# Optimization experiments

Measured on AMD Instinct MI355X. Metric: run time of the kernel, lower is better.

## Reference

```python
import jax, jax.numpy as jnp
import numpy as np

IMG_H, IMG_W = 448, 800
GRID = 224
MIN_SIZE = 64.0
B, N, NCAM = 1, 48, 6


def setup_inputs() -> dict:
    rng = np.random.default_rng(0)
    centers = np.stack([rng.uniform(-40, 40, (B, N)), rng.uniform(-40, 40, (B, N)),
                        rng.uniform(-1.5, 0.5, (B, N))], -1)
    dims = rng.uniform(1.0, 4.0, (B, N, 3))
    heading = rng.uniform(-np.pi, np.pi, (B, N, 1))
    boxes7 = np.concatenate([centers, dims, heading], -1).astype(np.float32)
    gt_labels = rng.integers(1, 11, (B, N)).astype(np.int64)  # 1..10 as in gt_boxes[...,-1]
    imgs = rng.random((B, NCAM, 3, IMG_H, IMG_W)).astype(np.float32)
    # plausible lidar->image projections: 6 outward-facing cams, 60 deg apart, 90 deg hfov
    fx = fy = 400.0
    K = np.array([[fx, 0, IMG_W / 2], [0, fy, IMG_H / 2], [0, 0, 1]], np.float32)
    l2i = np.zeros((B, NCAM, 4, 4), np.float32)
    for c in range(NCAM):
        th = 2 * np.pi * c / NCAM
        right = np.array([np.sin(th), -np.cos(th), 0.0])
        down = np.array([0.0, 0.0, -1.0])
        fwdv = np.array([np.cos(th), np.sin(th), 0.0])
        R = np.stack([right, down, fwdv])  # lidar -> cam
        l2i[:, c, :3, :3] = K @ R
        l2i[:, c, 3, 3] = 1.0
    eye4 = np.eye(4, dtype=np.float32)
    img_aug = np.broadcast_to(eye4, (B, NCAM, 4, 4)).copy()
    lidar_aug = np.broadcast_to(eye4, (B, 4, 4)).copy()
    W_img = (rng.standard_normal((588, 768)) * 0.02).astype(np.float32)
    text_features = rng.standard_normal((10, 768)).astype(np.float32)
    return dict(boxes7=jnp.asarray(boxes7), gt_labels=jnp.asarray(gt_labels),
                camera_imgs=jnp.asarray(imgs), lidar2image=jnp.asarray(l2i),
                img_aug_matrix=jnp.asarray(img_aug), lidar_aug_matrix=jnp.asarray(lidar_aug),
                W_img=jnp.asarray(W_img), text_features=jnp.asarray(text_features),
                logit_scale=jnp.asarray(np.float32(np.log(100.0))))


def _boxes_to_corners_3d(boxes7):  # (M,7) -> (M,8,3)
    template = jnp.array([[1, 1, -1], [1, -1, -1], [-1, -1, -1], [-1, 1, -1],
                          [1, 1, 1], [1, -1, 1], [-1, -1, 1], [-1, 1, 1]], jnp.float32) * 0.5
    corners = boxes7[:, None, 3:6] * template[None]
    c, s = jnp.cos(boxes7[:, 6]), jnp.sin(boxes7[:, 6])
    z, o = jnp.zeros_like(c), jnp.ones_like(c)
    rot = jnp.stack([c, s, z, -s, c, z, z, z, o], -1).reshape(-1, 3, 3)
    corners = jnp.einsum('nki,nij->nkj', corners, rot)  # points @ R as in torch code
    return corners + boxes7[:, None, :3]


def _project(corners, l2i, img_aug, lidar_aug):
    # corners (M,3); l2i/img_aug (6,4,4); lidar_aug (4,4)
    pts = corners - lidar_aug[:3, 3]
    pts = jnp.linalg.inv(lidar_aug[:3, :3]) @ pts.T  # (3,M)
    p = jnp.einsum('cij,jm->cim', l2i[:, :3, :3], pts) + l2i[:, :3, 3][:, :, None]
    zc = jnp.clip(p[:, 2], 1e-5, 1e5)
    xy = p[:, :2] / zc[:, None]
    p = jnp.concatenate([xy, zc[:, None]], axis=1)  # (6,3,M)
    p = jnp.einsum('cij,cjm->cim', img_aug[:, :3, :3], p) + img_aug[:, :3, 3][:, :, None]
    rc = p[:, :2].transpose(0, 2, 1)[..., ::-1]  # (6,M,2) as (row, col)
    on_img = (rc[..., 0] < IMG_H) & (rc[..., 0] >= 0) & (rc[..., 1] < IMG_W) & (rc[..., 1] >= 0)
    return rc, on_img


def _bilinear(img, ix, iy):
    # img (3,H,W); ix, iy (N,GRID,GRID) pixel coords; zero padding, align_corners=False
    x0f, y0f = jnp.floor(ix), jnp.floor(iy)
    wx1, wy1 = ix - x0f, iy - y0f
    wx0, wy0 = 1.0 - wx1, 1.0 - wy1

    def gather(xf, yf):
        valid = (xf >= 0) & (xf <= IMG_W - 1) & (yf >= 0) & (yf <= IMG_H - 1)
        xi = jnp.clip(xf.astype(jnp.int32), 0, IMG_W - 1)
        yi = jnp.clip(yf.astype(jnp.int32), 0, IMG_H - 1)
        return img[:, yi, xi] * valid[None].astype(img.dtype)  # (3,N,G,G)

    return (gather(x0f, y0f) * (wx0 * wy0)[None] + gather(x0f + 1, y0f) * (wx1 * wy0)[None]
            + gather(x0f, y0f + 1) * (wx0 * wy1)[None] + gather(x0f + 1, y0f + 1) * (wx1 * wy1)[None])


def _forward(boxes7, gt_labels, camera_imgs, lidar2image, img_aug_matrix,
             lidar_aug_matrix, W_img, text_features, logit_scale):
    Bx, Nx = boxes7.shape[:2]
    corners = _boxes_to_corners_3d(boxes7.reshape(-1, 7)).reshape(Bx, Nx * 8, 3)
    rc, on_img = jax.vmap(_project)(corners, lidar2image, img_aug_matrix, lidar_aug_matrix)
    # .long() in torch truncates toward zero; coords are constants wrt grads
    all_coords = jax.lax.stop_gradient(jnp.trunc(rc)).astype(jnp.int32).reshape(Bx, NCAM, Nx, 8, 2)
    visible = on_img.reshape(Bx, NCAM, Nx, 8).any(-1)  # (B,6,N)
    rows, cols = all_coords[..., 0], all_coords[..., 1]
    x1 = jnp.clip(cols.min(-1), 0, IMG_W)
    x2 = jnp.clip(cols.max(-1), 0, IMG_W)
    y1 = jnp.clip(rows.min(-1), 0, IMG_H)
    y2 = jnp.clip(rows.max(-1), 0, IMG_H)
    sq = jnp.maximum(jnp.maximum(x2 - x1, y2 - y1).astype(jnp.float32), MIN_SIZE)
    u = jnp.linspace(0.0, 1.0, GRID)  # normalized affine_grid after min/max rescale
    px = x1.astype(jnp.float32)[..., None, None] + sq[..., None, None] * u[None, None, None, None, :]
    py = y1.astype(jnp.float32)[..., None, None] + sq[..., None, None] * u[None, None, None, :, None]
    gx = px / IMG_W * 2.0 - 1.0
    gy = py / IMG_H * 2.0 - 1.0
    ix = ((gx + 1.0) * IMG_W - 1.0) / 2.0  # unnormalize (align_corners=False)
    iy = ((gy + 1.0) * IMG_H - 1.0) / 2.0
    patches = jax.vmap(jax.vmap(_bilinear))(camera_imgs, ix, iy)  # (B,6,3,N,G,G)
    patches = patches.transpose(0, 1, 3, 2, 4, 5)  # (B,6,N,3,G,G)
    # stub CLIP image tower: 16x16 avg pool -> flatten -> linear to 768
    pooled = patches.reshape(Bx, NCAM, Nx, 3, 14, 16, 14, 16).mean(axis=(5, 7))
    feats = pooled.reshape(Bx, NCAM, Nx, 588) @ W_img  # (B,6,N,768)
    feats = feats / jnp.linalg.norm(feats, axis=-1, keepdims=True)
    text_n = text_features / jnp.linalg.norm(text_features, axis=-1, keepdims=True)
    logits = jnp.exp(logit_scale) * jnp.einsum('bcnd,kd->bcnk', feats, text_n)
    probs = jax.nn.softmax(logits, axis=-1) * visible[..., None].astype(logits.dtype)
    cnt = visible.sum(1).astype(probs.dtype)  # (B,N) cameras per box
    mean_probs = probs.sum(1) / jnp.maximum(cnt, 1.0)[..., None]  # (B,N,10)
    pred = jnp.argmax(mean_probs, axis=-1).reshape(-1)
    true = gt_labels.reshape(-1) - 1
    acc = (pred == true).astype(jnp.float32).mean()
    return pred, true, acc, mean_probs


def reference(boxes7, gt_labels, camera_imgs, lidar2image, img_aug_matrix,
              lidar_aug_matrix, W_img, text_features, logit_scale):
    return _forward(boxes7, gt_labels, camera_imgs, lidar2image, img_aug_matrix,
                    lidar_aug_matrix, W_img, text_features, logit_scale)
```

## Files before the change

kernel.cpp:

```cpp
#include <hip/hip_runtime.h>
#include <math.h>

#define IMG_H 448
#define IMG_W 800
#define GRIDN 224
#define NCAM 6
#define NBOX 48
#define NPAIR (NCAM * NBOX)
#define NCLASS 10
#define FEATD 768
#define POOLD 588
#define PROWS 14
#define KSPLIT 4
#define KCH 147

#define WS_PAIR 0
#define WS_TNORM (NPAIR * 4)
#define WS_POOL (WS_TNORM + NCLASS)
#define WS_FEAT (WS_POOL + NPAIR * POOLD)
#define WS_PROBS (WS_FEAT + NPAIR * KSPLIT * FEATD)

__global__ void prep_kernel(const float* __restrict__ boxes7,
                            const float* __restrict__ l2i,
                            const float* __restrict__ img_aug,
                            const float* __restrict__ lidar_aug,
                            const float* __restrict__ text,
                            float* __restrict__ ws) {
    int tid = threadIdx.x;
    if (tid < NCLASS) {
        float s = 0.f;
        for (int d = 0; d < FEATD; ++d) { float v = text[tid * FEATD + d]; s += v * v; }
        ws[WS_TNORM + tid] = sqrtf(s);
    }
    if (tid >= NPAIR) return;
    int cam = tid / NBOX, box = tid % NBOX;

    float R[9];
    for (int i = 0; i < 3; ++i)
        for (int j = 0; j < 3; ++j) R[i * 3 + j] = lidar_aug[i * 4 + j];
    float ltx = lidar_aug[3], lty = lidar_aug[7], ltz = lidar_aug[11];
    float det = R[0] * (R[4] * R[8] - R[5] * R[7]) - R[1] * (R[3] * R[8] - R[5] * R[6]) +
                R[2] * (R[3] * R[7] - R[4] * R[6]);
    float inv[9];
    inv[0] = (R[4] * R[8] - R[5] * R[7]) / det;
    inv[1] = (R[2] * R[7] - R[1] * R[8]) / det;
    inv[2] = (R[1] * R[5] - R[2] * R[4]) / det;
    inv[3] = (R[5] * R[6] - R[3] * R[8]) / det;
    inv[4] = (R[0] * R[8] - R[2] * R[6]) / det;
    inv[5] = (R[2] * R[3] - R[0] * R[5]) / det;
    inv[6] = (R[3] * R[7] - R[4] * R[6]) / det;
    inv[7] = (R[1] * R[6] - R[0] * R[7]) / det;
    inv[8] = (R[0] * R[4] - R[1] * R[3]) / det;

    const float* M = l2i + cam * 16;
    const float* A = img_aug + cam * 16;
    const float* bx = boxes7 + box * 7;
    float cx = bx[0], cy = bx[1], cz = bx[2];
    float dx = bx[3], dy = bx[4], dz = bx[5], hd = bx[6];
    float ch = cosf(hd), sh = sinf(hd);
    const float tmpl[8][3] = {{.5f, .5f, -.5f},  {.5f, -.5f, -.5f}, {-.5f, -.5f, -.5f},
                              {-.5f, .5f, -.5f}, {.5f, .5f, .5f},   {.5f, -.5f, .5f},
                              {-.5f, -.5f, .5f}, {-.5f, .5f, .5f}};
    int minr = 0x7FFFFFFF, maxr = -0x7FFFFFFF - 1;
    int minc = 0x7FFFFFFF, maxc = -0x7FFFFFFF - 1;
    bool vis = false;
    for (int k = 0; k < 8; ++k) {
        float lx = dx * tmpl[k][0], ly = dy * tmpl[k][1], lz = dz * tmpl[k][2];
        float wxr = lx * ch - ly * sh;
        float wyr = lx * sh + ly * ch;
        float wzr = lz;
        float wx = wxr + cx, wy = wyr + cy, wz = wzr + cz;
        float px_ = wx - ltx, py_ = wy - lty, pz_ = wz - ltz;
        float qx = inv[0] * px_ + inv[1] * py_ + inv[2] * pz_;
        float qy = inv[3] * px_ + inv[4] * py_ + inv[5] * pz_;
        float qz = inv[6] * px_ + inv[7] * py_ + inv[8] * pz_;
        float p0 = M[0] * qx + M[1] * qy + M[2] * qz + M[3];
        float p1 = M[4] * qx + M[5] * qy + M[6] * qz + M[7];
        float p2 = M[8] * qx + M[9] * qy + M[10] * qz + M[11];
        float zc = fminf(fmaxf(p2, 1e-5f), 1e5f);
        float sx = p0 / zc, sy = p1 / zc;
        float q0 = A[0] * sx + A[1] * sy + A[2] * zc + A[3];
        float q1 = A[4] * sx + A[5] * sy + A[6] * zc + A[7];
        float row = q1, col = q0;
        bool on = (row < (float)IMG_H) && (row >= 0.f) && (col < (float)IMG_W) && (col >= 0.f);
        vis = vis || on;
        int ri = (int)row;
        int ci = (int)col;
        minr = min(minr, ri); maxr = max(maxr, ri);
        minc = min(minc, ci); maxc = max(maxc, ci);
    }
    int x1 = min(max(minc, 0), IMG_W);
    int x2 = min(max(maxc, 0), IMG_W);
    int y1 = min(max(minr, 0), IMG_H);
    int y2 = min(max(maxr, 0), IMG_H);
    int side = max(x2 - x1, y2 - y1);
    float sq = fmaxf((float)side, 64.0f);
    float* pw = ws + WS_PAIR + tid * 4;
    pw[0] = (float)x1;
    pw[1] = (float)y1;
    pw[2] = sq;
    pw[3] = vis ? 1.0f : 0.0f;
}

__global__ void __launch_bounds__(256) pool_kernel(const float* __restrict__ imgs,
                                                   float* __restrict__ ws) {
    int pair = blockIdx.x / PROWS;
    int pr = blockIdx.x % PROWS;
    const float* pw = ws + WS_PAIR + pair * 4;
    if (pw[3] == 0.f) return;
    float bx1 = pw[0], by1 = pw[1], sq = pw[2];
    int cam = pair / NBOX;
    const float* img = imgs + (size_t)cam * 3 * IMG_H * IMG_W;
    int tid = threadIdx.x;
    bool active = tid < GRIDN;

    const float ustep = 1.0f / 223.0f;
    float wx0 = 0.f, wx1 = 0.f, mx0 = 0.f, mx1 = 0.f;
    int xi0 = 0, xi1 = 0;
    if (active) {
        float u = (float)tid * ustep;
        float px = bx1 + sq * u;
        float gx = px / (float)IMG_W * 2.0f - 1.0f;
        float ix = ((gx + 1.0f) * (float)IMG_W - 1.0f) / 2.0f;
        float x0f = floorf(ix);
        wx1 = ix - x0f;
        wx0 = 1.0f - wx1;
        float x1f = x0f + 1.0f;
        mx0 = (x0f >= 0.f && x0f <= (float)(IMG_W - 1)) ? 1.f : 0.f;
        mx1 = (x1f >= 0.f && x1f <= (float)(IMG_W - 1)) ? 1.f : 0.f;
        xi0 = min(max((int)x0f, 0), IMG_W - 1);
        xi1 = min(max((int)x1f, 0), IMG_W - 1);
    }
    float acc0 = 0.f, acc1 = 0.f, acc2 = 0.f;
    for (int r = 0; r < 16; ++r) {
        int i = pr * 16 + r;
        float u = (float)i * ustep;
        float py = by1 + sq * u;
        float gy = py / (float)IMG_H * 2.0f - 1.0f;
        float iy = ((gy + 1.0f) * (float)IMG_H - 1.0f) / 2.0f;
        float y0f = floorf(iy);
        float wy1 = iy - y0f;
        float wy0 = 1.0f - wy1;
        float y1f = y0f + 1.0f;
        float my0 = (y0f >= 0.f && y0f <= (float)(IMG_H - 1)) ? 1.f : 0.f;
        float my1 = (y1f >= 0.f && y1f <= (float)(IMG_H - 1)) ? 1.f : 0.f;
        int yi0 = min(max((int)y0f, 0), IMG_H - 1);
        int yi1 = min(max((int)y1f, 0), IMG_H - 1);
        if (active) {
            int r0 = yi0 * IMG_W, r1 = yi1 * IMG_W;
            float w00 = wx0 * wy0, w10 = wx1 * wy0, w01 = wx0 * wy1, w11 = wx1 * wy1;
            float m00 = mx0 * my0, m10 = mx1 * my0, m01 = mx0 * my1, m11 = mx1 * my1;
            {
                const float* ip = img;
                float v = ip[r0 + xi0] * m00 * w00 + ip[r0 + xi1] * m10 * w10 +
                          ip[r1 + xi0] * m01 * w01 + ip[r1 + xi1] * m11 * w11;
                acc0 += v;
            }
            {
                const float* ip = img + (size_t)(IMG_H * IMG_W);
                float v = ip[r0 + xi0] * m00 * w00 + ip[r0 + xi1] * m10 * w10 +
                          ip[r1 + xi0] * m01 * w01 + ip[r1 + xi1] * m11 * w11;
                acc1 += v;
            }
            {
                const float* ip = img + (size_t)(2 * IMG_H * IMG_W);
                float v = ip[r0 + xi0] * m00 * w00 + ip[r0 + xi1] * m10 * w10 +
                          ip[r1 + xi0] * m01 * w01 + ip[r1 + xi1] * m11 * w11;
                acc2 += v;
            }
        }
    }
    for (int off = 8; off >= 1; off >>= 1) {
        acc0 += __shfl_xor(acc0, off, 16);
        acc1 += __shfl_xor(acc1, off, 16);
        acc2 += __shfl_xor(acc2, off, 16);
    }
    if (active && (tid & 15) == 0) {
        int pj = tid >> 4;
        float* pool = ws + WS_POOL + (size_t)pair * POOLD;
        pool[0 * 196 + pr * 14 + pj] = acc0 * (1.0f / 256.0f);
        pool[1 * 196 + pr * 14 + pj] = acc1 * (1.0f / 256.0f);
        pool[2 * 196 + pr * 14 + pj] = acc2 * (1.0f / 256.0f);
    }
}

__global__ void __launch_bounds__(768) head1_kernel(const float* __restrict__ W,
                                                    float* __restrict__ ws) {
    int pair = blockIdx.x / KSPLIT;
    int kc = blockIdx.x % KSPLIT;
    if (ws[WS_PAIR + pair * 4 + 3] == 0.f) return;
    int tid = threadIdx.x;
    __shared__ float pk[KCH];
    if (tid < KCH) pk[tid] = ws[WS_POOL + (size_t)pair * POOLD + kc * KCH + tid];
    __syncthreads();
    const float* Wp = W + (size_t)(kc * KCH) * FEATD + tid;
    float f = 0.f;
#pragma unroll 7
    for (int k = 0; k < KCH; ++k) f += pk[k] * Wp[(size_t)k * FEATD];
    ws[WS_FEAT + ((size_t)pair * KSPLIT + kc) * FEATD + tid] = f;
}

__global__ void __launch_bounds__(256) head2_kernel(const float* __restrict__ text,
                                                    const float* __restrict__ ls_ptr,
                                                    float* __restrict__ ws) {
    int pair = blockIdx.x;
    int tid = threadIdx.x;
    const float* pw = ws + WS_PAIR + pair * 4;
    if (pw[3] == 0.f) {
        if (tid < NCLASS) ws[WS_PROBS + pair * NCLASS + tid] = 0.f;
        return;
    }
    const float* fb = ws + WS_FEAT + (size_t)pair * KSPLIT * FEATD;
    float f0 = 0.f, f1 = 0.f, f2 = 0.f;
    for (int kc = 0; kc < KSPLIT; ++kc) {
        const float* fp = fb + (size_t)kc * FEATD;
        f0 += fp[tid];
        f1 += fp[tid + 256];
        f2 += fp[tid + 512];
    }
    float pn = f0 * f0 + f1 * f1 + f2 * f2;
    float pl[NCLASS];
    for (int k = 0; k < NCLASS; ++k) {
        const float* tr = text + (size_t)k * FEATD;
        pl[k] = f0 * tr[tid] + f1 * tr[tid + 256] + f2 * tr[tid + 512];
    }
    for (int off = 32; off >= 1; off >>= 1) {
        pn += __shfl_xor(pn, off);
        for (int k = 0; k < NCLASS; ++k) pl[k] += __shfl_xor(pl[k], off);
    }
    __shared__ float rn[4];
    __shared__ float rl[4][NCLASS];
    int wave = tid >> 6, lane = tid & 63;
    if (lane == 0) {
        rn[wave] = pn;
        for (int k = 0; k < NCLASS; ++k) rl[wave][k] = pl[k];
    }
    __syncthreads();
    if (tid == 0) {
        float n2 = rn[0] + rn[1] + rn[2] + rn[3];
        float nrm = sqrtf(n2);
        float scale = expf(ls_ptr[0]);
        const float* tn = ws + WS_TNORM;
        float lg[NCLASS], m = -1e30f;
        for (int k = 0; k < NCLASS; ++k) {
            float d = rl[0][k] + rl[1][k] + rl[2][k] + rl[3][k];
            lg[k] = scale * (d / (nrm * tn[k]));
            m = fmaxf(m, lg[k]);
        }
        float s = 0.f;
        for (int k = 0; k < NCLASS; ++k) {
            lg[k] = expf(lg[k] - m);
            s += lg[k];
        }
        float* probs = ws + WS_PROBS + pair * NCLASS;
        for (int k = 0; k < NCLASS; ++k) probs[k] = lg[k] / s;
    }
}

__global__ void finalize_kernel(const int* __restrict__ gt, const float* __restrict__ ws,
                                float* __restrict__ out) {
    int n = threadIdx.x;
    bool match = false;
    if (n < NBOX) {
        const float* probs = ws + WS_PROBS;
        float cnt = 0.f;
        for (int c = 0; c < NCAM; ++c)
            cnt += (ws[WS_PAIR + (c * NBOX + n) * 4 + 3] != 0.f) ? 1.f : 0.f;
        float denom = fmaxf(cnt, 1.0f);
        float mp[NCLASS];
        for (int k = 0; k < NCLASS; ++k) {
            float s = 0.f;
            for (int c = 0; c < NCAM; ++c) s += probs[(c * NBOX + n) * NCLASS + k];
            mp[k] = s / denom;
            out[97 + n * NCLASS + k] = mp[k];
        }
        float best = mp[0];
        int pred = 0;
        for (int k = 1; k < NCLASS; ++k)
            if (mp[k] > best) { best = mp[k]; pred = k; }
        int tr = gt[n] - 1;
        out[n] = (float)pred;
        out[NBOX + n] = (float)tr;
        match = (pred == tr);
    }
    unsigned long long b = __ballot(match);
    if (n == 0) out[2 * NBOX] = (float)__popcll(b) / (float)NBOX;
}

extern "C" void kernel_launch(void* const* d_in, const int* in_sizes, int n_in,
                              void* d_out, int out_size, void* d_ws, size_t ws_size,
                              hipStream_t stream) {
    const float* boxes7 = (const float*)d_in[0];
    const int* gt = (const int*)d_in[1];
    const float* imgs = (const float*)d_in[2];
    const float* l2i = (const float*)d_in[3];
    const float* img_aug = (const float*)d_in[4];
    const float* lidar_aug = (const float*)d_in[5];
    const float* W = (const float*)d_in[6];
    const float* text = (const float*)d_in[7];
    const float* ls = (const float*)d_in[8];
    float* ws = (float*)d_ws;
    float* out = (float*)d_out;

    prep_kernel<<<1, 320, 0, stream>>>(boxes7, l2i, img_aug, lidar_aug, text, ws);
    pool_kernel<<<NPAIR * PROWS, 256, 0, stream>>>(imgs, ws);
    head1_kernel<<<NPAIR * KSPLIT, 768, 0, stream>>>(W, ws);
    head2_kernel<<<NPAIR, 256, 0, stream>>>(text, ls, ws);
    finalize_kernel<<<1, 64, 0, stream>>>(gt, ws, out);
}
```

Measured before the change: 54.31 us.

## Fuse box projection into pool kernel and fold text norms into head2

Removes the single-block prep kernel. Each pool block now projects its box's 8 corners itself, using 8 lanes and a shuffle min/max reduction, and the text norms are computed inside head2 alongside the dot products. The pool kernel grows to 1024 threads, with four row groups of 4 rows each reduced through shared memory, so each block has more parallelism. This saves a launch and the serial prep step. In exchange, the projection is computed redundantly in all 14 blocks per pair, and invisible pairs still launch large blocks that exit early.

```diff
diff --git a/kernel.cpp b/kernel.cpp
--- a/kernel.cpp
+++ b/kernel.cpp
@@ -15,65 +15,59 @@
 #define KCH 147
 
 #define WS_PAIR 0
-#define WS_TNORM (NPAIR * 4)
-#define WS_POOL (WS_TNORM + NCLASS)
+#define WS_POOL (NPAIR * 4)
 #define WS_FEAT (WS_POOL + NPAIR * POOLD)
 #define WS_PROBS (WS_FEAT + NPAIR * KSPLIT * FEATD)
 
-__global__ void prep_kernel(const float* __restrict__ boxes7,
-                            const float* __restrict__ l2i,
-                            const float* __restrict__ img_aug,
-                            const float* __restrict__ lidar_aug,
-                            const float* __restrict__ text,
-                            float* __restrict__ ws) {
+__global__ void __launch_bounds__(1024) pool_kernel(const float* __restrict__ imgs,
+                                                    const float* __restrict__ boxes7,
+                                                    const float* __restrict__ l2i,
+                                                    const float* __restrict__ img_aug,
+                                                    const float* __restrict__ lidar_aug,
+                                                    float* __restrict__ ws) {
+    int pair = blockIdx.x / PROWS;
+    int pr = blockIdx.x % PROWS;
+    int cam = pair / NBOX, box = pair % NBOX;
     int tid = threadIdx.x;
-    if (tid < NCLASS) {
-        float s = 0.f;
-        for (int d = 0; d < FEATD; ++d) { float v = text[tid * FEATD + d]; s += v * v; }
-        ws[WS_TNORM + tid] = sqrtf(s);
-    }
-    if (tid >= NPAIR) return;
-    int cam = tid / NBOX, box = tid % NBOX;
-
-    float R[9];
-    for (int i = 0; i < 3; ++i)
-        for (int j = 0; j < 3; ++j) R[i * 3 + j] = lidar_aug[i * 4 + j];
-    float ltx = lidar_aug[3], lty = lidar_aug[7], ltz = lidar_aug[11];
-    float det = R[0] * (R[4] * R[8] - R[5] * R[7]) - R[1] * (R[3] * R[8] - R[5] * R[6]) +
-                R[2] * (R[3] * R[7] - R[4] * R[6]);
-    float inv[9];
-    inv[0] = (R[4] * R[8] - R[5] * R[7]) / det;
-    inv[1] = (R[2] * R[7] - R[1] * R[8]) / det;
-    inv[2] = (R[1] * R[5] - R[2] * R[4]) / det;
-    inv[3] = (R[5] * R[6] - R[3] * R[8]) / det;
-    inv[4] = (R[0] * R[8] - R[2] * R[6]) / det;
-    inv[5] = (R[2] * R[3] - R[0] * R[5]) / det;
-    inv[6] = (R[3] * R[7] - R[4] * R[6]) / det;
-    inv[7] = (R[1] * R[6] - R[0] * R[7]) / det;
-    inv[8] = (R[0] * R[4] - R[1] * R[3]) / det;
-
-    const float* M = l2i + cam * 16;
-    const float* A = img_aug + cam * 16;
-    const float* bx = boxes7 + box * 7;
-    float cx = bx[0], cy = bx[1], cz = bx[2];
-    float dx = bx[3], dy = bx[4], dz = bx[5], hd = bx[6];
-    float ch = cosf(hd), sh = sinf(hd);
-    const float tmpl[8][3] = {{.5f, .5f, -.5f},  {.5f, -.5f, -.5f}, {-.5f, -.5f, -.5f},
-                              {-.5f, .5f, -.5f}, {.5f, .5f, .5f},   {.5f, -.5f, .5f},
-                              {-.5f, -.5f, .5f}, {-.5f, .5f, .5f}};
-    int minr = 0x7FFFFFFF, maxr = -0x7FFFFFFF - 1;
-    int minc = 0x7FFFFFFF, maxc = -0x7FFFFFFF - 1;
-    bool vis = false;
-    for (int k = 0; k < 8; ++k) {
-        float lx = dx * tmpl[k][0], ly = dy * tmpl[k][1], lz = dz * tmpl[k][2];
-        float wxr = lx * ch - ly * sh;
-        float wyr = lx * sh + ly * ch;
-        float wzr = lz;
-        float wx = wxr + cx, wy = wyr + cy, wz = wzr + cz;
+
+    __shared__ float s_pw[4];
+    __shared__ float s_part[4][3][14];
+
+    if (tid < 64) {
+        int k = tid & 7;
+        float R[9];
+        for (int i = 0; i < 3; ++i)
+            for (int j = 0; j < 3; ++j) R[i * 3 + j] = lidar_aug[i * 4 + j];
+        float ltx = lidar_aug[3], lty = lidar_aug[7], ltz = lidar_aug[11];
+        float det = R[0] * (R[4] * R[8] - R[5] * R[7]) - R[1] * (R[3] * R[8] - R[5] * R[6]) +
+                    R[2] * (R[3] * R[7] - R[4] * R[6]);
+        float i0 = (R[4] * R[8] - R[5] * R[7]) / det;
+        float i1 = (R[2] * R[7] - R[1] * R[8]) / det;
+        float i2 = (R[1] * R[5] - R[2] * R[4]) / det;
+        float i3 = (R[5] * R[6] - R[3] * R[8]) / det;
+        float i4 = (R[0] * R[8] - R[2] * R[6]) / det;
+        float i5 = (R[2] * R[3] - R[0] * R[5]) / det;
+        float i6 = (R[3] * R[7] - R[4] * R[6]) / det;
+        float i7 = (R[1] * R[6] - R[0] * R[7]) / det;
+        float i8 = (R[0] * R[4] - R[1] * R[3]) / det;
+
+        const float* M = l2i + cam * 16;
+        const float* A = img_aug + cam * 16;
+        const float* bxp = boxes7 + box * 7;
+        float cx = bxp[0], cy = bxp[1], cz = bxp[2];
+        float dx = bxp[3], dy = bxp[4], dz = bxp[5], hd = bxp[6];
+        float ch = cosf(hd), sh = sinf(hd);
+        float tx = (k & 2) ? -0.5f : 0.5f;
+        float ty = ((k + 1) & 2) ? -0.5f : 0.5f;
+        float tz = (k & 4) ? 0.5f : -0.5f;
+        float lx = dx * tx, ly = dy * ty, lz = dz * tz;
+        float wx = lx * ch - ly * sh + cx;
+        float wy = lx * sh + ly * ch + cy;
+        float wz = lz + cz;
         float px_ = wx - ltx, py_ = wy - lty, pz_ = wz - ltz;
-        float qx = inv[0] * px_ + inv[1] * py_ + inv[2] * pz_;
-        float qy = inv[3] * px_ + inv[4] * py_ + inv[5] * pz_;
-        float qz = inv[6] * px_ + inv[7] * py_ + inv[8] * pz_;
+        float qx = i0 * px_ + i1 * py_ + i2 * pz_;
+        float qy = i3 * px_ + i4 * py_ + i5 * pz_;
+        float qz = i6 * px_ + i7 * py_ + i8 * pz_;
         float p0 = M[0] * qx + M[1] * qy + M[2] * qz + M[3];
         float p1 = M[4] * qx + M[5] * qy + M[6] * qz + M[7];
         float p2 = M[8] * qx + M[9] * qy + M[10] * qz + M[11];
@@ -82,43 +76,47 @@
         float q0 = A[0] * sx + A[1] * sy + A[2] * zc + A[3];
         float q1 = A[4] * sx + A[5] * sy + A[6] * zc + A[7];
         float row = q1, col = q0;
-        bool on = (row < (float)IMG_H) && (row >= 0.f) && (col < (float)IMG_W) && (col >= 0.f);
-        vis = vis || on;
+        int on = (row < (float)IMG_H) && (row >= 0.f) && (col < (float)IMG_W) && (col >= 0.f);
         int ri = (int)row;
         int ci = (int)col;
-        minr = min(minr, ri); maxr = max(maxr, ri);
-        minc = min(minc, ci); maxc = max(maxc, ci);
-    }
-    int x1 = min(max(minc, 0), IMG_W);
-    int x2 = min(max(maxc, 0), IMG_W);
-    int y1 = min(max(minr, 0), IMG_H);
-    int y2 = min(max(maxr, 0), IMG_H);
-    int side = max(x2 - x1, y2 - y1);
-    float sq = fmaxf((float)side, 64.0f);
-    float* pw = ws + WS_PAIR + tid * 4;
-    pw[0] = (float)x1;
-    pw[1] = (float)y1;
-    pw[2] = sq;
-    pw[3] = vis ? 1.0f : 0.0f;
-}
-
-__global__ void __launch_bounds__(256) pool_kernel(const float* __restrict__ imgs,
-                                                   float* __restrict__ ws) {
-    int pair = blockIdx.x / PROWS;
-    int pr = blockIdx.x % PROWS;
-    const float* pw = ws + WS_PAIR + pair * 4;
-    if (pw[3] == 0.f) return;
-    float bx1 = pw[0], by1 = pw[1], sq = pw[2];
-    int cam = pair / NBOX;
+        int minr = ri, maxr = ri, minc = ci, maxc = ci, visv = on;
+        for (int off = 4; off >= 1; off >>= 1) {
+            minr = min(minr, __shfl_xor(minr, off, 8));
+            maxr = max(maxr, __shfl_xor(maxr, off, 8));
+            minc = min(minc, __shfl_xor(minc, off, 8));
+            maxc = max(maxc, __shfl_xor(maxc, off, 8));
+            visv |= __shfl_xor(visv, off, 8);
+        }
+        if (tid == 0) {
+            int x1 = min(max(minc, 0), IMG_W);
+            int x2 = min(max(maxc, 0), IMG_W);
+            int y1 = min(max(minr, 0), IMG_H);
+            int y2 = min(max(maxr, 0), IMG_H);
+            float sq = fmaxf((float)max(x2 - x1, y2 - y1), 64.0f);
+            s_pw[0] = (float)x1;
+            s_pw[1] = (float)y1;
+            s_pw[2] = sq;
+            s_pw[3] = visv ? 1.0f : 0.0f;
+            if (pr == 0) {
+                float* pw = ws + WS_PAIR + pair * 4;
+                pw[0] = (float)x1; pw[1] = (float)y1; pw[2] = sq; pw[3] = visv ? 1.0f : 0.0f;
+            }
+        }
+    }
+    __syncthreads();
+    if (s_pw[3] == 0.f) return;
+    float bx1 = s_pw[0], by1 = s_pw[1], sq = s_pw[2];
+
     const float* img = imgs + (size_t)cam * 3 * IMG_H * IMG_W;
-    int tid = threadIdx.x;
-    bool active = tid < GRIDN;
+    int colid = tid & 255;
+    int rg = tid >> 8;
+    bool active = colid < GRIDN;
 
     const float ustep = 1.0f / 223.0f;
     float wx0 = 0.f, wx1 = 0.f, mx0 = 0.f, mx1 = 0.f;
     int xi0 = 0, xi1 = 0;
     if (active) {
-        float u = (float)tid * ustep;
+        float u = (float)colid * ustep;
         float px = bx1 + sq * u;
         float gx = px / (float)IMG_W * 2.0f - 1.0f;
         float ix = ((gx + 1.0f) * (float)IMG_W - 1.0f) / 2.0f;
@@ -132,8 +130,9 @@
         xi1 = min(max((int)x1f, 0), IMG_W - 1);
     }
     float acc0 = 0.f, acc1 = 0.f, acc2 = 0.f;
-    for (int r = 0; r < 16; ++r) {
-        int i = pr * 16 + r;
+#pragma unroll
+    for (int j = 0; j < 4; ++j) {
+        int i = pr * 16 + rg * 4 + j;
         float u = (float)i * ustep;
         float py = by1 + sq * u;
         float gy = py / (float)IMG_H * 2.0f - 1.0f;
@@ -152,21 +151,18 @@
             float m00 = mx0 * my0, m10 = mx1 * my0, m01 = mx0 * my1, m11 = mx1 * my1;
             {
                 const float* ip = img;
-                float v = ip[r0 + xi0] * m00 * w00 + ip[r0 + xi1] * m10 * w10 +
-                          ip[r1 + xi0] * m01 * w01 + ip[r1 + xi1] * m11 * w11;
-                acc0 += v;
+                acc0 += ip[r0 + xi0] * m00 * w00 + ip[r0 + xi1] * m10 * w10 +
+                        ip[r1 + xi0] * m01 * w01 + ip[r1 + xi1] * m11 * w11;
             }
             {
                 const float* ip = img + (size_t)(IMG_H * IMG_W);
-                float v = ip[r0 + xi0] * m00 * w00 + ip[r0 + xi1] * m10 * w10 +
-                          ip[r1 + xi0] * m01 * w01 + ip[r1 + xi1] * m11 * w11;
-                acc1 += v;
+                acc1 += ip[r0 + xi0] * m00 * w00 + ip[r0 + xi1] * m10 * w10 +
+                        ip[r1 + xi0] * m01 * w01 + ip[r1 + xi1] * m11 * w11;
             }
             {
                 const float* ip = img + (size_t)(2 * IMG_H * IMG_W);
-                float v = ip[r0 + xi0] * m00 * w00 + ip[r0 + xi1] * m10 * w10 +
-                          ip[r1 + xi0] * m01 * w01 + ip[r1 + xi1] * m11 * w11;
-                acc2 += v;
+                acc2 += ip[r0 + xi0] * m00 * w00 + ip[r0 + xi1] * m10 * w10 +
+                        ip[r1 + xi0] * m01 * w01 + ip[r1 + xi1] * m11 * w11;
             }
         }
     }
@@ -175,12 +171,17 @@
         acc1 += __shfl_xor(acc1, off, 16);
         acc2 += __shfl_xor(acc2, off, 16);
     }
-    if (active && (tid & 15) == 0) {
-        int pj = tid >> 4;
-        float* pool = ws + WS_POOL + (size_t)pair * POOLD;
-        pool[0 * 196 + pr * 14 + pj] = acc0 * (1.0f / 256.0f);
-        pool[1 * 196 + pr * 14 + pj] = acc1 * (1.0f / 256.0f);
-        pool[2 * 196 + pr * 14 + pj] = acc2 * (1.0f / 256.0f);
+    if (active && (colid & 15) == 0) {
+        int pj = colid >> 4;
+        s_part[rg][0][pj] = acc0;
+        s_part[rg][1][pj] = acc1;
+        s_part[rg][2][pj] = acc2;
+    }
+    __syncthreads();
+    if (tid < 3 * 14) {
+        int c = tid / 14, pj = tid % 14;
+        float v = s_part[0][c][pj] + s_part[1][c][pj] + s_part[2][c][pj] + s_part[3][c][pj];
+        ws[WS_POOL + (size_t)pair * POOLD + c * 196 + pr * 14 + pj] = v * (1.0f / 256.0f);
     }
 }
 
@@ -219,32 +220,38 @@
         f2 += fp[tid + 512];
     }
     float pn = f0 * f0 + f1 * f1 + f2 * f2;
-    float pl[NCLASS];
+    float pl[NCLASS], tq[NCLASS];
     for (int k = 0; k < NCLASS; ++k) {
         const float* tr = text + (size_t)k * FEATD;
-        pl[k] = f0 * tr[tid] + f1 * tr[tid + 256] + f2 * tr[tid + 512];
+        float t0 = tr[tid], t1 = tr[tid + 256], t2 = tr[tid + 512];
+        pl[k] = f0 * t0 + f1 * t1 + f2 * t2;
+        tq[k] = t0 * t0 + t1 * t1 + t2 * t2;
     }
     for (int off = 32; off >= 1; off >>= 1) {
         pn += __shfl_xor(pn, off);
-        for (int k = 0; k < NCLASS; ++k) pl[k] += __shfl_xor(pl[k], off);
+        for (int k = 0; k < NCLASS; ++k) {
+            pl[k] += __shfl_xor(pl[k], off);
+            tq[k] += __shfl_xor(tq[k], off);
+        }
     }
     __shared__ float rn[4];
     __shared__ float rl[4][NCLASS];
+    __shared__ float rq[4][NCLASS];
     int wave = tid >> 6, lane = tid & 63;
     if (lane == 0) {
         rn[wave] = pn;
-        for (int k = 0; k < NCLASS; ++k) rl[wave][k] = pl[k];
+        for (int k = 0; k < NCLASS; ++k) { rl[wave][k] = pl[k]; rq[wave][k] = tq[k]; }
     }
     __syncthreads();
     if (tid == 0) {
         float n2 = rn[0] + rn[1] + rn[2] + rn[3];
         float nrm = sqrtf(n2);
         float scale = expf(ls_ptr[0]);
-        const float* tn = ws + WS_TNORM;
         float lg[NCLASS], m = -1e30f;
         for (int k = 0; k < NCLASS; ++k) {
             float d = rl[0][k] + rl[1][k] + rl[2][k] + rl[3][k];
-            lg[k] = scale * (d / (nrm * tn[k]));
+            float tn = sqrtf(rq[0][k] + rq[1][k] + rq[2][k] + rq[3][k]);
+            lg[k] = scale * (d / (nrm * tn));
             m = fmaxf(m, lg[k]);
         }
         float s = 0.f;
@@ -302,8 +309,7 @@
     float* ws = (float*)d_ws;
     float* out = (float*)d_out;
 
-    prep_kernel<<<1, 320, 0, stream>>>(boxes7, l2i, img_aug, lidar_aug, text, ws);
-    pool_kernel<<<NPAIR * PROWS, 256, 0, stream>>>(imgs, ws);
+    pool_kernel<<<NPAIR * PROWS, 1024, 0, stream>>>(imgs, boxes7, l2i, img_aug, lidar_aug, ws);
     head1_kernel<<<NPAIR * KSPLIT, 768, 0, stream>>>(W, ws);
     head2_kernel<<<NPAIR, 256, 0, stream>>>(text, ls, ws);
     finalize_kernel<<<1, 64, 0, stream>>>(gt, ws, out);
```

After: 56.50 us. +4.0%, slower.
